# Kernel tuning notes

Hardware: AMD Instinct MI355X
Metric: run time of the kernel (lower is better)

Reference implementation:

```python
import jax, jax.numpy as jnp
import numpy as np

BS, SEQ, HID = 2, 2048, 1024
HEADS, BLOCK = 16, 64
HEAD_DIM = HID // HEADS


def setup_inputs() -> dict:
    key = jax.random.key(0)
    ks = jax.random.split(key, 5)
    s = 1.0 / np.sqrt(HID)
    return {
        "hidden_states": jax.random.normal(ks[0], (BS, SEQ, HID), jnp.float32),
        "Wq": jax.random.normal(ks[1], (HID, HID), jnp.float32) * s,
        "bq": jnp.zeros((HID,), jnp.float32),
        "Wk": jax.random.normal(ks[2], (HID, HID), jnp.float32) * s,
        "bk": jnp.zeros((HID,), jnp.float32),
        "Wv": jax.random.normal(ks[3], (HID, HID), jnp.float32) * s,
        "bv": jnp.zeros((HID,), jnp.float32),
        "Wo": jax.random.normal(ks[4], (HID, HID), jnp.float32) * s,
        "bo": jnp.zeros((HID,), jnp.float32),
    }


def reference(hidden_states, Wq, bq, Wk, bk, Wv, bv, Wo, bo):
    b, s, _ = hidden_states.shape
    # torch Linear: y = x @ W.T + b
    q = (hidden_states @ Wq.T + bq).reshape(b, s, HEADS, HEAD_DIM)
    k = (hidden_states @ Wk.T + bk).reshape(b, s, HEADS, HEAD_DIM)
    v = (hidden_states @ Wv.T + bv).reshape(b, s, HEADS, HEAD_DIM)
    scale = 1.0 / np.sqrt(HEAD_DIM).astype(np.float32)
    scores = jnp.einsum("bqhd,bkhd->bhqk", q, k) * scale  # [B,H,S,S]
    # block-level causal mask: kv block index <= query block index
    blk = jnp.arange(s) // BLOCK
    mask = blk[None, :] <= blk[:, None]  # [S,S]
    scores = jnp.where(mask[None, None], scores, jnp.finfo(scores.dtype).min)
    attn = jax.nn.softmax(scores, axis=-1)
    out = jnp.einsum("bhqk,bkhd->bqhd", attn, v).reshape(b, s, HID)
    return out @ Wo.T + bo
```

## Files before the change

### kernel.cpp

```cpp
#include <hip/hip_runtime.h>

#define BS 2
#define SEQ 2048
#define HID 1024
#define HEADS 16
#define HDIM 64
#define MTOT (BS * SEQ)

#define QSCALE 0.18033688f

typedef __bf16 bf16x8 __attribute__((ext_vector_type(8)));
typedef float floatx4 __attribute__((ext_vector_type(4)));
typedef short short8 __attribute__((ext_vector_type(8)));
typedef unsigned short u16x4 __attribute__((ext_vector_type(4)));
typedef unsigned int u32x2 __attribute__((ext_vector_type(2)));

__device__ __forceinline__ floatx4 mfma16x16x32bf16(short8 a, short8 b, floatx4 c) {
    return __builtin_amdgcn_mfma_f32_16x16x32_bf16(
        __builtin_bit_cast(bf16x8, a), __builtin_bit_cast(bf16x8, b), c, 0, 0, 0);
}

__device__ __forceinline__ unsigned short f2bf(float f) {
    unsigned int u = __builtin_bit_cast(unsigned int, f);
    u += 0x7fffu + ((u >> 16) & 1u);
    return (unsigned short)(u >> 16);
}

__device__ __forceinline__ unsigned int cvt_pk_bf16(float lo, float hi) {
    unsigned int r;
    asm("v_cvt_pk_bf16_f32 %0, %1, %2" : "=v"(r) : "v"(lo), "v"(hi));
    return r;
}

__device__ __forceinline__ float fast_exp2(float x) {
#if __has_builtin(__builtin_amdgcn_exp2f)
    return __builtin_amdgcn_exp2f(x);
#else
    return __expf(x * 0.6931471805599453f);
#endif
}

#define GLOAD_LDS16(gsrc, ldst)                                                   \
    __builtin_amdgcn_global_load_lds(                                             \
        (const __attribute__((address_space(1))) void*)(gsrc),                    \
        (__attribute__((address_space(3))) void*)(ldst), 16, 0, 0)

__global__ __launch_bounds__(256) void cvt5(
    const float* __restrict__ X, const float* __restrict__ Wq,
    const float* __restrict__ Wk, const float* __restrict__ Wv,
    const float* __restrict__ Wo, unsigned short* __restrict__ dst)
{
    const int y = blockIdx.y;
    const float* src = (y == 0) ? X : (y == 1) ? Wq : (y == 2) ? Wk : (y == 3) ? Wv : Wo;
    const size_t base = (y == 0) ? 0 : (size_t)(4u << 20) + (size_t)(y - 1) * (1u << 20);
    const int n4 = (y == 0) ? (1 << 20) : (1 << 18);
    const float scale = (y == 1) ? QSCALE : 1.0f;
    int i = blockIdx.x * 256 + threadIdx.x;
    if (i >= n4) return;
    floatx4 v = *(const floatx4*)(src + (size_t)i * 4);
    v *= scale;
    unsigned int p0 = (unsigned int)f2bf(v[0]) | ((unsigned int)f2bf(v[1]) << 16);
    unsigned int p1 = (unsigned int)f2bf(v[2]) | ((unsigned int)f2bf(v[3]) << 16);
    u32x2 pk = {p0, p1};
    *(u32x2*)(dst + base + (size_t)i * 4) = pk;
}

__global__ __launch_bounds__(256) void gemm_qkv(
    const unsigned short* __restrict__ X,
    const unsigned short* __restrict__ W0, const unsigned short* __restrict__ W1,
    const unsigned short* __restrict__ W2,
    const float* __restrict__ B0, const float* __restrict__ B1,
    const float* __restrict__ B2,
    unsigned short* __restrict__ out_bf)
{
    __shared__ __align__(16) unsigned short sA[64 * 32];
    __shared__ __align__(16) unsigned short sB[3][128 * 32];

    const int tid  = threadIdx.x;
    const int m0   = blockIdx.x * 64;
    const int n0   = blockIdx.y * 128;
    const int lane = tid & 63, w = tid >> 6;
    const int l16  = lane & 15, grp = lane >> 4;
    const int wm   = w & 1, wn = w >> 1;

    const unsigned short* Wz[3] = {W0, W1, W2};

    floatx4 acc[3][2][4];
#pragma unroll
    for (int z = 0; z < 3; ++z)
#pragma unroll
        for (int i = 0; i < 2; ++i)
#pragma unroll
            for (int j = 0; j < 4; ++j) acc[z][i][j] = (floatx4){0.f, 0.f, 0.f, 0.f};

    auto stage = [&](int kb) {
        const int kcol = kb * 32;
        {
            int row = tid >> 2, c8 = (tid & 3) * 8;
            GLOAD_LDS16(X + (size_t)(m0 + row) * HID + kcol + c8, &sA[tid * 8]);
        }
#pragma unroll
        for (int i = 0; i < 6; ++i) {
            int g2 = tid + i * 256;
            int z = g2 >> 9, g3 = g2 & 511;
            int row = g3 >> 2, c8 = (g3 & 3) * 8;
            GLOAD_LDS16(Wz[z] + (size_t)(n0 + row) * HID + kcol + c8, &sB[z][g3 * 8]);
        }
    };

    stage(0);
    for (int kb = 0; kb < 32; ++kb) {
        __syncthreads();
        short8 af[2], bfr[3][4];
#pragma unroll
        for (int t = 0; t < 2; ++t)
            af[t] = *(const short8*)&sA[(wm * 32 + t * 16 + l16) * 32 + grp * 8];
#pragma unroll
        for (int z = 0; z < 3; ++z)
#pragma unroll
            for (int t = 0; t < 4; ++t)
                bfr[z][t] = *(const short8*)&sB[z][(wn * 64 + t * 16 + l16) * 32 + grp * 8];
        __syncthreads();
        if (kb + 1 < 32) stage(kb + 1);
#pragma unroll
        for (int mt = 0; mt < 2; ++mt)
#pragma unroll
            for (int nt = 0; nt < 4; ++nt) {
                acc[0][mt][nt] = mfma16x16x32bf16(bfr[0][nt], af[mt], acc[0][mt][nt]);
                acc[1][mt][nt] = mfma16x16x32bf16(bfr[1][nt], af[mt], acc[1][mt][nt]);
                acc[2][mt][nt] = mfma16x16x32bf16(af[mt], bfr[2][nt], acc[2][mt][nt]);
            }
    }

    const int hidx = (n0 + wn * 64) >> 6;
    {
#pragma unroll
        for (int nt = 0; nt < 4; ++nt) {
            int dbase = nt * 16 + grp * 4;
            floatx4 b4 = *(const floatx4*)&B0[n0 + wn * 64 + dbase];
            b4 *= QSCALE;
#pragma unroll
            for (int mt = 0; mt < 2; ++mt) {
                int m = m0 + wm * 32 + mt * 16 + l16;
                int bidx = m >> 11, s = m & (SEQ - 1);
                u32x2 pk;
                pk[0] = cvt_pk_bf16(acc[0][mt][nt][0] + b4[0], acc[0][mt][nt][1] + b4[1]);
                pk[1] = cvt_pk_bf16(acc[0][mt][nt][2] + b4[2], acc[0][mt][nt][3] + b4[3]);
                *(u32x2*)&out_bf[
                    ((((size_t)bidx * HEADS + hidx) * SEQ + s) * HDIM + dbase)] = pk;
            }
        }
    }
    {
        const size_t outz = (size_t)MTOT * HID;
        const int bidx = m0 >> 11;
        const int kvb  = (m0 & (SEQ - 1)) >> 6;
        const size_t hbase = outz + ((size_t)bidx * HEADS + hidx) * SEQ * HDIM;
        const int grpf = grp >> 1, j0 = (grp & 1) * 4;
#pragma unroll
        for (int nt = 0; nt < 4; ++nt) {
            floatx4 b4 = *(const floatx4*)&B1[n0 + wn * 64 + nt * 16 + grp * 4];
#pragma unroll
            for (int mt = 0; mt < 2; ++mt) {
                u32x2 pk;
                pk[0] = cvt_pk_bf16(acc[1][mt][nt][0] + b4[0], acc[1][mt][nt][1] + b4[1]);
                pk[1] = cvt_pk_bf16(acc[1][mt][nt][2] + b4[2], acc[1][mt][nt][3] + b4[3]);
                size_t F = hbase
                    + (size_t)((((kvb * 4 + (wm * 2 + mt)) * 2 + (nt >> 1)) * 512)
                    + ((((nt & 1) * 2 + grpf) * 16 + l16) * 8) + j0);
                *(u32x2*)&out_bf[F] = pk;
            }
        }
    }
    {
        const size_t outz = (size_t)2 * ((size_t)MTOT * HID);
        const int bidx = m0 >> 11;
        const int kvb  = (m0 & (SEQ - 1)) >> 6;
        const size_t hbase = outz + ((size_t)bidx * HEADS + hidx) * SEQ * HDIM;
        const int j0 = (grp & 1) * 4;
#pragma unroll
        for (int nt = 0; nt < 4; ++nt) {
            float bias = B2[n0 + wn * 64 + nt * 16 + l16];
#pragma unroll
            for (int mt = 0; mt < 2; ++mt) {
                u32x2 pk;
                pk[0] = cvt_pk_bf16(acc[2][mt][nt][0] + bias, acc[2][mt][nt][1] + bias);
                pk[1] = cvt_pk_bf16(acc[2][mt][nt][2] + bias, acc[2][mt][nt][3] + bias);
                size_t F = hbase + (size_t)((((kvb * 4 + nt) * 2 + wm) * 512)
                    + (((mt * 2 + (grp >> 1)) * 16 + l16) * 8) + j0);
                *(u32x2*)&out_bf[F] = pk;
            }
        }
    }
}

template <int BM, int BN>
__global__ __launch_bounds__(256) void gemm_out(
    const unsigned short* __restrict__ X, const unsigned short* __restrict__ W,
    const float* __restrict__ Bb, float* __restrict__ out_f)
{
    constexpr int MT = BM / 32, NT = BN / 32;
    constexpr int NCH = (BM + BN) * 4;
    __shared__ __align__(16) unsigned short sA[BM * 32];
    __shared__ __align__(16) unsigned short sB[BN * 32];

    const int tid  = threadIdx.x;
    const int m0   = blockIdx.x * BM;
    const int n0   = blockIdx.y * BN;
    const int lane = tid & 63, w = tid >> 6;
    const int l16  = lane & 15, grp = lane >> 4;
    const int wm   = w & 1, wn = w >> 1;

    floatx4 acc[MT][NT];
#pragma unroll
    for (int i = 0; i < MT; ++i)
#pragma unroll
        for (int j = 0; j < NT; ++j) acc[i][j] = (floatx4){0.f, 0.f, 0.f, 0.f};

    auto stage = [&](int kb) {
        const int kcol = kb * 32;
#pragma unroll
        for (int i = 0; i < NCH / 256; ++i) {
            int g = tid + i * 256;
            if (g < BM * 4) {
                int row = g >> 2, c8 = (g & 3) * 8;
                GLOAD_LDS16(X + (size_t)(m0 + row) * HID + kcol + c8, &sA[g * 8]);
            } else {
                int g2 = g - BM * 4;
                int row = g2 >> 2, c8 = (g2 & 3) * 8;
                GLOAD_LDS16(W + (size_t)(n0 + row) * HID + kcol + c8, &sB[g2 * 8]);
            }
        }
    };

    stage(0);
    for (int kb = 0; kb < 32; ++kb) {
        __syncthreads();
        short8 af[MT], bfr[NT];
#pragma unroll
        for (int t = 0; t < MT; ++t)
            af[t] = *(const short8*)&sA[(wm * (BM / 2) + t * 16 + l16) * 32 + grp * 8];
#pragma unroll
        for (int t = 0; t < NT; ++t)
            bfr[t] = *(const short8*)&sB[(wn * (BN / 2) + t * 16 + l16) * 32 + grp * 8];
        __syncthreads();
        if (kb + 1 < 32) stage(kb + 1);
#pragma unroll
        for (int mt = 0; mt < MT; ++mt)
#pragma unroll
            for (int nt = 0; nt < NT; ++nt)
                acc[mt][nt] = mfma16x16x32bf16(af[mt], bfr[nt], acc[mt][nt]);
    }

#pragma unroll
    for (int nt = 0; nt < NT; ++nt) {
        int n = n0 + wn * (BN / 2) + nt * 16 + l16;
        float bias = Bb[n];
#pragma unroll
        for (int mt = 0; mt < MT; ++mt)
#pragma unroll
            for (int r = 0; r < 4; ++r) {
                int m = m0 + wm * (BM / 2) + mt * 16 + grp * 4 + r;
                out_f[(size_t)m * HID + n] = acc[mt][nt][r] + bias;
            }
    }
}

__global__ __launch_bounds__(256) void attn_kernel(
    const unsigned short* __restrict__ Qw, const unsigned short* __restrict__ Kf,
    const unsigned short* __restrict__ Vf, unsigned short* __restrict__ X2)
{
    __shared__ __align__(16) unsigned short Ps[4][16][72];

    const int wg = blockIdx.x;
    const int xcd = wg & 7, k = wg >> 3;
    const int bh  = (k >> 4) * 8 + xcd;
    const int pairj = k & 15;
    const int tid = threadIdx.x;
    const int quarter = tid >> 6;
    const int b = bh >> 4, h = bh & 15;

    const int lane = tid & 63;
    const int l16  = lane & 15, grp = lane >> 4;

    const size_t head = ((size_t)b * HEADS + h) * (size_t)SEQ * HDIM;
    const unsigned short* Kh = Kf + head;
    const unsigned short* Vh = Vf + head;

    short8 ka[4][2], kbuf[4][2], vf[4][2];

    auto loadK = [&](short8 (&kf)[4][2], int kb) {
#pragma unroll
        for (int nt = 0; nt < 4; ++nt)
#pragma unroll
            for (int ks = 0; ks < 2; ++ks)
                kf[nt][ks] = *(const short8*)(Kh +
                    (size_t)(((kb * 4 + nt) * 2 + ks) * 512) + lane * 8);
    };

#pragma unroll 1
    for (int phase = 0; phase < 2; ++phase) {
        const int qblk = phase ? (31 - pairj) : pairj;
        const int nkb  = qblk + 1;
        const int q0   = qblk * 64 + quarter * 16;

        short8 qf[2];
#pragma unroll
        for (int ks = 0; ks < 2; ++ks)
            qf[ks] = *(const short8*)(Qw + head +
                (size_t)(q0 + l16) * HDIM + ks * 32 + grp * 8);

        floatx4 o[4];
#pragma unroll
        for (int i = 0; i < 4; ++i) o[i] = (floatx4){0.f, 0.f, 0.f, 0.f};
        float mi = -1e30f, li = 0.f;

        auto process = [&](short8 (&kfc)[4][2], short8 (&kfn)[4][2], int kb) {
            {
#pragma unroll
                for (int nt = 0; nt < 4; ++nt)
#pragma unroll
                    for (int ks = 0; ks < 2; ++ks)
                        vf[nt][ks] = *(const short8*)(Vh +
                            (size_t)(((kb * 4 + nt) * 2 + ks) * 512) + lane * 8);
            }
            floatx4 sv[4];
            __builtin_amdgcn_s_setprio(1);
#pragma unroll
            for (int nt = 0; nt < 4; ++nt) {
                floatx4 zz = (floatx4){0.f, 0.f, 0.f, 0.f};
                zz = mfma16x16x32bf16(kfc[nt][0], qf[0], zz);
                zz = mfma16x16x32bf16(kfc[nt][1], qf[1], zz);
                sv[nt] = zz;
            }
            __builtin_amdgcn_s_setprio(0);
            if (kb + 1 < nkb) loadK(kfn, kb + 1);

            float m01 = fmaxf(fmaxf(sv[0][0], sv[0][1]), fmaxf(sv[0][2], sv[0][3]));
            float m23 = fmaxf(fmaxf(sv[1][0], sv[1][1]), fmaxf(sv[1][2], sv[1][3]));
            float m45 = fmaxf(fmaxf(sv[2][0], sv[2][1]), fmaxf(sv[2][2], sv[2][3]));
            float m67 = fmaxf(fmaxf(sv[3][0], sv[3][1]), fmaxf(sv[3][2], sv[3][3]));
            float mx = fmaxf(fmaxf(m01, m23), fmaxf(m45, m67));
            mx = fmaxf(mx, __shfl_xor(mx, 16));
            mx = fmaxf(mx, __shfl_xor(mx, 32));
            if (!__all(mx - mi <= 8.f)) {
                float mn = fmaxf(mi, mx);
                float alpha = fast_exp2(mi - mn);
                mi = mn;
                li *= alpha;
#pragma unroll
                for (int dt = 0; dt < 4; ++dt) o[dt] *= alpha;
            }
            float rs = 0.f;
#pragma unroll
            for (int nt = 0; nt < 4; ++nt) {
                floatx4 p;
#pragma unroll
                for (int r = 0; r < 4; ++r) p[r] = fast_exp2(sv[nt][r] - mi);
                sv[nt] = p;
                rs += (p[0] + p[1]) + (p[2] + p[3]);
            }
            rs += __shfl_xor(rs, 16);
            rs += __shfl_xor(rs, 32);
            li += rs;

#pragma unroll
            for (int nt = 0; nt < 4; ++nt) {
                u32x2 pk;
                pk[0] = cvt_pk_bf16(sv[nt][0], sv[nt][1]);
                pk[1] = cvt_pk_bf16(sv[nt][2], sv[nt][3]);
                *(u32x2*)&Ps[quarter][l16][nt * 16 + grp * 4] = pk;
            }

            short8 pf0 = *(const short8*)&Ps[quarter][l16][grp * 8];
            short8 pf1 = *(const short8*)&Ps[quarter][l16][32 + grp * 8];
            __builtin_amdgcn_s_setprio(1);
#pragma unroll
            for (int dt = 0; dt < 4; ++dt) {
                o[dt] = mfma16x16x32bf16(vf[dt][0], pf0, o[dt]);
                o[dt] = mfma16x16x32bf16(vf[dt][1], pf1, o[dt]);
            }
            __builtin_amdgcn_s_setprio(0);
        };

        loadK(ka, 0);
        int kb = 0;
        while (true) {
            process(ka, kbuf, kb);
            if (++kb >= nkb) break;
            process(kbuf, ka, kb);
            if (++kb >= nkb) break;
        }

        float inv = 1.0f / li;
        int srow = q0 + l16;
#pragma unroll
        for (int dt = 0; dt < 4; ++dt) {
            u32x2 pk;
            pk[0] = cvt_pk_bf16(o[dt][0] * inv, o[dt][1] * inv);
            pk[1] = cvt_pk_bf16(o[dt][2] * inv, o[dt][3] * inv);
            *(u32x2*)&X2[((size_t)b * SEQ + srow) * HID +
                         h * HDIM + dt * 16 + grp * 4] = pk;
        }
    }
}

extern "C" void kernel_launch(void* const* d_in, const int* in_sizes, int n_in,
                              void* d_out, int out_size, void* d_ws, size_t ws_size,
                              hipStream_t stream) {
    int iX, iWq, ibq, iWk, ibk, iWv, ibv, iWo, ibo;
    if (in_sizes[0] == MTOT * HID) {
        iX = 0; iWq = 1; ibq = 2; iWk = 3; ibk = 4; iWv = 5; ibv = 6; iWo = 7; ibo = 8;
    } else {
        iWk = 0; iWo = 1; iWq = 2; iWv = 3; ibk = 4; ibo = 5; ibq = 6; ibv = 7; iX = 8;
    }
    const float* X  = (const float*)d_in[iX];
    const float* Wq = (const float*)d_in[iWq];
    const float* bq = (const float*)d_in[ibq];
    const float* Wk = (const float*)d_in[iWk];
    const float* bk = (const float*)d_in[ibk];
    const float* Wv = (const float*)d_in[iWv];
    const float* bv = (const float*)d_in[ibv];
    const float* Wo = (const float*)d_in[iWo];
    const float* bo = (const float*)d_in[ibo];
    float* out = (float*)d_out;

    unsigned short* ws = (unsigned short*)d_ws;
    const size_t T = (size_t)MTOT * HID;
    unsigned short* qw  = ws;
    unsigned short* kfr = ws + T;
    unsigned short* vfr = ws + 2 * T;
    unsigned short* x2  = ws + 3 * T;
    unsigned short* Xb  = ws + 4 * T;
    unsigned short* Wqb = Xb + T;
    unsigned short* Wkb = Wqb + (size_t)HID * HID;
    unsigned short* Wvb = Wkb + (size_t)HID * HID;
    unsigned short* Wob = Wvb + (size_t)HID * HID;

    cvt5<<<dim3(4096, 5), 256, 0, stream>>>(X, Wq, Wk, Wv, Wo, Xb);
    gemm_qkv<<<dim3(64, 8), 256, 0, stream>>>(
        Xb, Wqb, Wkb, Wvb, bq, bk, bv, qw);
    attn_kernel<<<dim3(512), 256, 0, stream>>>(qw, kfr, vfr, x2);
    gemm_out<64, 128><<<dim3(64, 8), 256, 0, stream>>>(x2, Wob, bo, out);
}
```

Before: 191.9 us.

## Stage K/V blocks through double-buffered LDS shared by all four waves

Each of the four waves previously loaded its own copy of every K and V block from global memory into registers. The change has the whole workgroup cooperatively copy each 64-key K and V tile into LDS with direct global-to-LDS loads, double-buffered, and each wave then reads its fragments from LDS. This cuts redundant global and L2 traffic fourfold. In exchange it adds a __syncthreads per key block and LDS read latency.

```diff
diff --git a/kernel.cpp b/kernel.cpp
--- a/kernel.cpp
+++ b/kernel.cpp
@@ -270,6 +270,8 @@
     const unsigned short* __restrict__ Qw, const unsigned short* __restrict__ Kf,
     const unsigned short* __restrict__ Vf, unsigned short* __restrict__ X2)
 {
+    __shared__ __align__(16) unsigned short sK[2][4096];
+    __shared__ __align__(16) unsigned short sV[2][4096];
     __shared__ __align__(16) unsigned short Ps[4][16][72];
 
     const int wg = blockIdx.x;
@@ -287,15 +289,13 @@
     const unsigned short* Kh = Kf + head;
     const unsigned short* Vh = Vf + head;
 
-    short8 ka[4][2], kbuf[4][2], vf[4][2];
-
-    auto loadK = [&](short8 (&kf)[4][2], int kb) {
-#pragma unroll
-        for (int nt = 0; nt < 4; ++nt)
-#pragma unroll
-            for (int ks = 0; ks < 2; ++ks)
-                kf[nt][ks] = *(const short8*)(Kh +
-                    (size_t)(((kb * 4 + nt) * 2 + ks) * 512) + lane * 8);
+    auto stage = [&](int kb, int buf) {
+        const unsigned short* Ks = Kh + (size_t)kb * 4096;
+        const unsigned short* Vs = Vh + (size_t)kb * 4096;
+        GLOAD_LDS16(Ks + tid * 8,         &sK[buf][tid * 8]);
+        GLOAD_LDS16(Ks + (tid + 256) * 8, &sK[buf][(tid + 256) * 8]);
+        GLOAD_LDS16(Vs + tid * 8,         &sV[buf][tid * 8]);
+        GLOAD_LDS16(Vs + (tid + 256) * 8, &sV[buf][(tid + 256) * 8]);
     };
 
 #pragma unroll 1
@@ -315,26 +315,34 @@
         for (int i = 0; i < 4; ++i) o[i] = (floatx4){0.f, 0.f, 0.f, 0.f};
         float mi = -1e30f, li = 0.f;
 
-        auto process = [&](short8 (&kfc)[4][2], short8 (&kfn)[4][2], int kb) {
-            {
-#pragma unroll
-                for (int nt = 0; nt < 4; ++nt)
-#pragma unroll
-                    for (int ks = 0; ks < 2; ++ks)
-                        vf[nt][ks] = *(const short8*)(Vh +
-                            (size_t)(((kb * 4 + nt) * 2 + ks) * 512) + lane * 8);
-            }
+        __syncthreads();
+        stage(0, 0);
+
+#pragma unroll 1
+        for (int kb = 0; kb < nkb; ++kb) {
+            const int buf = kb & 1;
+            __syncthreads();
+
+            short8 kfr[4][2], vfr[4][2];
+#pragma unroll
+            for (int nt = 0; nt < 4; ++nt)
+#pragma unroll
+                for (int ks = 0; ks < 2; ++ks) {
+                    kfr[nt][ks] = *(const short8*)&sK[buf][(nt * 2 + ks) * 512 + lane * 8];
+                    vfr[nt][ks] = *(const short8*)&sV[buf][(nt * 2 + ks) * 512 + lane * 8];
+                }
+            if (kb + 1 < nkb) stage(kb + 1, buf ^ 1);
+
             floatx4 sv[4];
             __builtin_amdgcn_s_setprio(1);
 #pragma unroll
             for (int nt = 0; nt < 4; ++nt) {
                 floatx4 zz = (floatx4){0.f, 0.f, 0.f, 0.f};
-                zz = mfma16x16x32bf16(kfc[nt][0], qf[0], zz);
-                zz = mfma16x16x32bf16(kfc[nt][1], qf[1], zz);
+                zz = mfma16x16x32bf16(kfr[nt][0], qf[0], zz);
+                zz = mfma16x16x32bf16(kfr[nt][1], qf[1], zz);
                 sv[nt] = zz;
             }
             __builtin_amdgcn_s_setprio(0);
-            if (kb + 1 < nkb) loadK(kfn, kb + 1);
 
             float m01 = fmaxf(fmaxf(sv[0][0], sv[0][1]), fmaxf(sv[0][2], sv[0][3]));
             float m23 = fmaxf(fmaxf(sv[1][0], sv[1][1]), fmaxf(sv[1][2], sv[1][3]));
@@ -377,19 +385,10 @@
             __builtin_amdgcn_s_setprio(1);
 #pragma unroll
             for (int dt = 0; dt < 4; ++dt) {
-                o[dt] = mfma16x16x32bf16(vf[dt][0], pf0, o[dt]);
-                o[dt] = mfma16x16x32bf16(vf[dt][1], pf1, o[dt]);
+                o[dt] = mfma16x16x32bf16(vfr[dt][0], pf0, o[dt]);
+                o[dt] = mfma16x16x32bf16(vfr[dt][1], pf1, o[dt]);
             }
             __builtin_amdgcn_s_setprio(0);
-        };
-
-        loadK(ka, 0);
-        int kb = 0;
-        while (true) {
-            process(ka, kbuf, kb);
-            if (++kb >= nkb) break;
-            process(kbuf, ka, kb);
-            if (++kb >= nkb) break;
         }
 
         float inv = 1.0f / li;
```

Measured after the change: 192.1 us. About the same (+0.1%).
